# Optimization experiments

Hardware: AMD Instinct MI355X
Metric: run time of the kernel (lower is better)

The kernel has to match this reference:

```python
import jax, jax.numpy as jnp
import numpy as np

N_NODES = 50000
N_EDGES = 800000
IN_FEATS = 128
N_HIDDEN = 128
N_CLASSES = 16


def setup_inputs() -> dict:
    key = jax.random.key(0)
    ks = jax.random.split(key, 10)
    d = {
        'x': jax.random.normal(ks[0], (N_NODES, IN_FEATS), dtype=jnp.float32),
        'src': jax.random.randint(ks[1], (N_EDGES,), 0, N_NODES, dtype=jnp.int32),
        'dst': jax.random.randint(ks[2], (N_EDGES,), 0, N_NODES, dtype=jnp.int32),
    }
    sc = 1.0 / np.sqrt(N_HIDDEN)
    d['w_self0'] = jax.random.normal(ks[3], (IN_FEATS, N_HIDDEN), dtype=jnp.float32) * sc
    d['w_neigh0'] = jax.random.normal(ks[4], (IN_FEATS, N_HIDDEN), dtype=jnp.float32) * sc
    d['b0'] = jnp.zeros((N_HIDDEN,), dtype=jnp.float32)
    d['w_self1'] = jax.random.normal(ks[5], (N_HIDDEN, N_HIDDEN), dtype=jnp.float32) * sc
    d['w_neigh1'] = jax.random.normal(ks[6], (N_HIDDEN, N_HIDDEN), dtype=jnp.float32) * sc
    d['b1'] = jnp.zeros((N_HIDDEN,), dtype=jnp.float32)
    d['w_self2'] = jax.random.normal(ks[7], (N_HIDDEN, N_HIDDEN), dtype=jnp.float32) * sc
    d['w_neigh2'] = jax.random.normal(ks[8], (N_HIDDEN, N_HIDDEN), dtype=jnp.float32) * sc
    d['b2'] = jnp.zeros((N_HIDDEN,), dtype=jnp.float32)
    d['w_head'] = jax.random.normal(ks[9], (N_HIDDEN, N_CLASSES), dtype=jnp.float32) * sc
    d['b_head'] = jnp.zeros((N_CLASSES,), dtype=jnp.float32)
    return d


def _sage_conv(h, src, dst, inv_deg, w_self, w_neigh, b):
    # mean aggregator: gather src features, scatter-add to dst, divide by in-degree
    agg = jax.ops.segment_sum(h[src], dst, num_segments=N_NODES)  # [N, d]
    neigh = agg * inv_deg[:, None]
    return h @ w_self + neigh @ w_neigh + b


def reference(x, src, dst, w_self0, w_neigh0, b0, w_self1, w_neigh1, b1,
              w_self2, w_neigh2, b2, w_head, b_head):
    deg = jax.ops.segment_sum(jnp.ones((src.shape[0],), jnp.float32), dst,
                              num_segments=N_NODES)
    inv_deg = 1.0 / jnp.maximum(deg, 1.0)
    h = x  # dropout is identity in eval mode
    for (ws, wn, b) in ((w_self0, w_neigh0, b0),
                        (w_self1, w_neigh1, b1),
                        (w_self2, w_neigh2, b2)):
        h = jax.nn.relu(_sage_conv(h, src, dst, inv_deg, ws, wn, b))
    pls = jnp.mean(h, axis=0, keepdims=True)  # AvgPooling over single graph -> [1, n_hidden]
    score = pls @ w_head + b_head  # [1, n_classes]
    return (score, pls)
```

## Files before the change

### kernel.cpp

```cpp
#include <hip/hip_runtime.h>
#include <hip/hip_bf16.h>
#include <hip/hip_fp8.h>
#include <stdint.h>

#define NN 50000
#define NE 800000
#define F 128
#define NCLS 16
#define NB 196
#define BCAP 5120
#define PA_EPT 16

typedef __attribute__((ext_vector_type(8))) short short8;
typedef __attribute__((ext_vector_type(4))) float f32x4;
typedef __attribute__((ext_vector_type(2))) float f32x2;
typedef __attribute__((ext_vector_type(4))) unsigned int uint4v;

#define OB_COLSUM    0u
#define OB_BCUR      512u
#define OB_BBASE     1536u
#define OB_ROWSTART  4096u
#define OB_INVDEG    204800u
#define OB_PAIRS     409600u
#define OB_SRCS16    4423680u
#define OB_WT        6023680u
#define OB_XB        6220800u
#define OB_HB1       19020800u
#define OB_X8        31820800u
#define OB_F8A       38220800u
#define OB_NB        44620800u

__device__ __forceinline__ uint32_t swz_off(uint32_t row, uint32_t k) {
    uint32_t c = ((k >> 5) << 2) | ((k >> 2) & 3u);
    uint32_t b = (((k >> 4) & 1u) << 3) | ((k & 3u) << 1);
    return (row << 8) + (((c ^ (row & 15u)) << 4) | b);
}

__device__ __forceinline__ uint32_t pack_bf2(float a, float b) {
    __hip_bfloat16 l = __float2bfloat16(a), h = __float2bfloat16(b);
    return ((uint32_t)(*(uint16_t*)&h) << 16) | (uint32_t)(*(uint16_t*)&l);
}

__device__ __forceinline__ uint8_t f32_to_fp8(float v) {
#if __has_builtin(__builtin_amdgcn_cvt_pk_fp8_f32)
    return (uint8_t)(__builtin_amdgcn_cvt_pk_fp8_f32(v, 0.f, 0, false) & 0xff);
#else
    __hip_fp8_e4m3 t(v);
    return t.__x;
#endif
}

__device__ __forceinline__ uint32_t f32x4_to_fp8x4(float a, float b, float c, float d) {
#if __has_builtin(__builtin_amdgcn_cvt_pk_fp8_f32)
    int r = __builtin_amdgcn_cvt_pk_fp8_f32(a, b, 0, false);
    r = __builtin_amdgcn_cvt_pk_fp8_f32(c, d, r, true);
    return (uint32_t)r;
#else
    __hip_fp8_e4m3 ta(a), tb(b), tc(c), td(d);
    return (uint32_t)ta.__x | ((uint32_t)tb.__x << 8) | ((uint32_t)tc.__x << 16) | ((uint32_t)td.__x << 24);
#endif
}

__device__ __forceinline__ void fp8x4_to_f32(uint32_t d, float& f0, float& f1, float& f2, float& f3) {
#if __has_builtin(__builtin_amdgcn_cvt_pk_f32_fp8)
    f32x2 lo = __builtin_amdgcn_cvt_pk_f32_fp8((int)d, false);
    f32x2 hi = __builtin_amdgcn_cvt_pk_f32_fp8((int)d, true);
    f0 = lo.x; f1 = lo.y; f2 = hi.x; f3 = hi.y;
#else
    __hip_fp8_e4m3 t0, t1, t2, t3;
    t0.__x = (uint8_t)(d & 0xff); t1.__x = (uint8_t)((d >> 8) & 0xff);
    t2.__x = (uint8_t)((d >> 16) & 0xff); t3.__x = (uint8_t)((d >> 24) & 0xff);
    f0 = (float)t0; f1 = (float)t1; f2 = (float)t2; f3 = (float)t3;
#endif
}

__device__ __forceinline__ void gload16(const void* g, void* l) {
    __builtin_amdgcn_global_load_lds(
        (const __attribute__((address_space(1))) unsigned int*)g,
        (__attribute__((address_space(3))) unsigned int*)l, 16, 0, 0);
}

__global__ __launch_bounds__(256) void convert_x2(const float* __restrict__ x,
                                                  uint8_t* __restrict__ xb,
                                                  uint8_t* __restrict__ x8,
                                                  float* __restrict__ colsum,
                                                  int* __restrict__ bcur) {
    if (blockIdx.x == 0) {
        int tt = threadIdx.x;
        if (tt < 128) colsum[tt] = 0.f;
        if (tt < NB) bcur[tt] = tt * BCAP;
    }
    int t = blockIdx.x * 256 + threadIdx.x;
    uint32_t row = (uint32_t)t >> 5;
    uint32_t q = (uint32_t)t & 31u;
    float4 v = *(const float4*)(x + row * F + q * 4);
    uint32_t c = ((q >> 3) << 2) | (q & 3u);
    uint32_t hi = (q >> 2) & 1u;
    uint2 pk;
    pk.x = pack_bf2(v.x, v.y);
    pk.y = pack_bf2(v.z, v.w);
    *(uint2*)(xb + (row << 8) + (((c ^ (row & 15u)) << 4) | (hi << 3))) = pk;
    *(uint32_t*)(x8 + row * 128u + q * 4u) = f32x4_to_fp8x4(v.x, v.y, v.z, v.w);
}

__global__ __launch_bounds__(256) void prep_w(const float* __restrict__ w0, const float* __restrict__ w1,
                                              const float* __restrict__ w2, const float* __restrict__ w3,
                                              const float* __restrict__ w4, const float* __restrict__ w5,
                                              uint8_t* __restrict__ wt) {
    int m = blockIdx.y;
    const float* w = m == 0 ? w0 : m == 1 ? w1 : m == 2 ? w2 : m == 3 ? w3 : m == 4 ? w4 : w5;
    int t = blockIdx.x * 256 + threadIdx.x;
    int n = t >> 6;
    int k0 = (t & 63) << 1;
    uint32_t pk = pack_bf2(w[k0 * F + n], w[(k0 + 1) * F + n]);
    *(uint32_t*)(wt + (uint32_t)m * 32768u + swz_off((uint32_t)n, (uint32_t)k0)) = pk;
}

__global__ __launch_bounds__(256) void pass_a(const int* __restrict__ src,
                                              const int* __restrict__ dst,
                                              int* __restrict__ bcur,
                                              uint32_t* __restrict__ pairs) {
    __shared__ int cnt[NB];
    __shared__ int base_s[NB];
    int t = threadIdx.x;
    for (int i = t; i < NB; i += 256) cnt[i] = 0;
    __syncthreads();

    uint32_t pk[PA_EPT];
    int bk[PA_EPT];
    int e0 = blockIdx.x * (256 * PA_EPT) + t;
#pragma unroll
    for (int j = 0; j < PA_EPT; ++j) {
        int e = e0 + j * 256;
        if (e < NE) {
            int sv = src[e], dv = dst[e];
            bk[j] = dv >> 8;
            pk[j] = (uint32_t)sv | (((uint32_t)dv & 255u) << 16);
            atomicAdd(&cnt[bk[j]], 1);
        } else bk[j] = -1;
    }
    __syncthreads();
    for (int i = t; i < NB; i += 256) {
        if (cnt[i] > 0) base_s[i] = atomicAdd(&bcur[i], cnt[i]);
        cnt[i] = 0;
    }
    __syncthreads();
#pragma unroll
    for (int j = 0; j < PA_EPT; ++j) {
        if (bk[j] >= 0) {
            int pos = base_s[bk[j]] + atomicAdd(&cnt[bk[j]], 1);
            pairs[pos] = pk[j];
        }
    }
}

__global__ __launch_bounds__(256) void bucket_scan(const int* __restrict__ bcur,
                                                   int* __restrict__ bbase,
                                                   int* __restrict__ row_start) {
    __shared__ int s[256];
    int t = threadIdx.x;
    int fill = (t < NB) ? (bcur[t] - t * BCAP) : 0;
    s[t] = fill;
    __syncthreads();
    for (int off = 1; off < 256; off <<= 1) {
        int u = (t >= off) ? s[t - off] : 0;
        __syncthreads();
        s[t] += u;
        __syncthreads();
    }
    if (t < NB) bbase[t] = s[t] - fill;
    if (t == 0) row_start[NN] = NE;
}

__global__ __launch_bounds__(256) void pass_b(const uint32_t* __restrict__ pairs,
                                              const int* __restrict__ bcur,
                                              const int* __restrict__ bbase,
                                              int* __restrict__ row_start,
                                              float* __restrict__ inv_deg,
                                              unsigned short* __restrict__ srcs) {
    __shared__ int cnt[256];
    __shared__ int s[256];
    __shared__ int cur[256];
    int b = blockIdx.x, t = threadIdx.x;
    int in0 = b * BCAP;
    int fill = bcur[b] - in0;
    int out0 = bbase[b];
    cnt[t] = 0;
    __syncthreads();
    for (int i = t; i < fill; i += 256)
        atomicAdd(&cnt[pairs[in0 + i] >> 16], 1);
    __syncthreads();
    int v = cnt[t];
    s[t] = v;
    __syncthreads();
    for (int off = 1; off < 256; off <<= 1) {
        int u = (t >= off) ? s[t - off] : 0;
        __syncthreads();
        s[t] += u;
        __syncthreads();
    }
    int excl = s[t] - v;
    cur[t] = out0 + excl;
    int row = (b << 8) + t;
    if (row < NN) {
        row_start[row] = out0 + excl;
        inv_deg[row] = 1.0f / (float)(v > 1 ? v : 1);
    }
    __syncthreads();
    for (int i = t; i < fill; i += 256) {
        uint32_t p = pairs[in0 + i];
        int pos = atomicAdd(&cur[p >> 16], 1);
        srcs[pos] = (unsigned short)(p & 0xffffu);
    }
}

__global__ __launch_bounds__(256) void aggregate_f8(
        const uint8_t* __restrict__ hf8, const int* __restrict__ row_start,
        const unsigned short* __restrict__ srcs, const float* __restrict__ inv_deg,
        uint8_t* __restrict__ nb) {
    int node = blockIdx.x * 4 + (threadIdx.x >> 6);
    int l = threadIdx.x & 63;
    int g = l >> 4;
    uint32_t m = (uint32_t)(l & 15);
    const uint8_t* base = hf8 + m * 8u;
    int e0 = row_start[node], e1 = row_start[node + 1];
    float a0=0.f,a1=0.f,a2=0.f,a3=0.f,a4=0.f,a5=0.f,a6=0.f,a7=0.f;

    int e = e0 + g;
    for (; e + 4 < e1; e += 8) {
        uint32_t sa = srcs[e];
        uint32_t sb = srcs[e + 4];
        uint2 da = *(const uint2*)(base + ((uint32_t)sa << 7));
        uint2 db = *(const uint2*)(base + ((uint32_t)sb << 7));
        float f0, f1, f2, f3;
        fp8x4_to_f32(da.x, f0,f1,f2,f3); a0+=f0; a1+=f1; a2+=f2; a3+=f3;
        fp8x4_to_f32(da.y, f0,f1,f2,f3); a4+=f0; a5+=f1; a6+=f2; a7+=f3;
        fp8x4_to_f32(db.x, f0,f1,f2,f3); a0+=f0; a1+=f1; a2+=f2; a3+=f3;
        fp8x4_to_f32(db.y, f0,f1,f2,f3); a4+=f0; a5+=f1; a6+=f2; a7+=f3;
    }
    if (e < e1) {
        uint32_t sa = srcs[e];
        uint2 da = *(const uint2*)(base + ((uint32_t)sa << 7));
        float f0, f1, f2, f3;
        fp8x4_to_f32(da.x, f0,f1,f2,f3); a0+=f0; a1+=f1; a2+=f2; a3+=f3;
        fp8x4_to_f32(da.y, f0,f1,f2,f3); a4+=f0; a5+=f1; a6+=f2; a7+=f3;
    }
    a0 += __shfl_xor(a0, 16); a1 += __shfl_xor(a1, 16);
    a2 += __shfl_xor(a2, 16); a3 += __shfl_xor(a3, 16);
    a4 += __shfl_xor(a4, 16); a5 += __shfl_xor(a5, 16);
    a6 += __shfl_xor(a6, 16); a7 += __shfl_xor(a7, 16);
    a0 += __shfl_xor(a0, 32); a1 += __shfl_xor(a1, 32);
    a2 += __shfl_xor(a2, 32); a3 += __shfl_xor(a3, 32);
    a4 += __shfl_xor(a4, 32); a5 += __shfl_xor(a5, 32);
    a6 += __shfl_xor(a6, 32); a7 += __shfl_xor(a7, 32);

    if (g == 0) {
        float idg = inv_deg[node];
        uint2 w0, w1;
        w0.x = pack_bf2(a0 * idg, a1 * idg);
        w0.y = pack_bf2(a2 * idg, a3 * idg);
        w1.x = pack_bf2(a4 * idg, a5 * idg);
        w1.y = pack_bf2(a6 * idg, a7 * idg);
        uint32_t c1 = m >> 2;
        uint32_t h  = (m >> 1) & 1u;
        uint32_t ca = (c1 << 2) | ((2u * m) & 3u);
        uint32_t cb = (c1 << 2) | ((2u * m + 1u) & 3u);
        uint32_t rx = (uint32_t)node & 15u;
        char* rowp = (char*)nb + ((uint32_t)node << 8);
        *(uint2*)(rowp + (((ca ^ rx) << 4) | (h << 3))) = w0;
        *(uint2*)(rowp + (((cb ^ rx) << 4) | (h << 3))) = w1;
    }
}

__global__ __launch_bounds__(256) void gemm_mfma(
        const uint8_t* __restrict__ a_self, const uint8_t* __restrict__ a_neigh,
        const uint8_t* __restrict__ wt_self, const uint8_t* __restrict__ wt_neigh,
        const float* __restrict__ bias, uint8_t* __restrict__ hout,
        uint8_t* hout_f8, float* colsum) {
    __shared__ uint4v As4[1024];
    __shared__ uint4v Ws4[2048];
    __shared__ float cs[128];
    int tid = threadIdx.x;
    int lane = tid & 63, wave = tid >> 6;
    int rl = lane & 15, g = lane >> 4;
    int row0 = blockIdx.x * 64;

    f32x4 acc[8];
    f32x4 z = {0.f, 0.f, 0.f, 0.f};
#pragma unroll
    for (int nt = 0; nt < 8; ++nt) acc[nt] = z;

    const char* AsB = (const char*)As4;
    const char* WsB = (const char*)Ws4;

#pragma unroll
    for (int pass = 0; pass < 2; ++pass) {
        if (pass) __syncthreads();
        const uint4v* ga = (const uint4v*)((pass ? a_neigh : a_self) + (size_t)row0 * 256);
        const uint4v* gw = (const uint4v*)(pass ? wt_neigh : wt_self);
#pragma unroll
        for (int i = 0; i < 4; ++i) gload16(&ga[tid + i * 256], &As4[tid + i * 256]);
#pragma unroll
        for (int i = 0; i < 8; ++i) gload16(&gw[tid + i * 256], &Ws4[tid + i * 256]);
        __syncthreads();
#pragma unroll
        for (int ks = 0; ks < 4; ++ks) {
            int chunk = ((ks << 2) | g) ^ rl;
            short8 a = *(const short8*)(AsB + ((wave * 16 + rl) << 8) + (chunk << 4));
#pragma unroll
            for (int nt = 0; nt < 8; ++nt) {
                short8 bb = *(const short8*)(WsB + ((nt * 16 + rl) << 8) + (chunk << 4));
                acc[nt] = __builtin_amdgcn_mfma_f32_16x16x32_bf16(a, bb, acc[nt], 0, 0, 0);
            }
        }
    }

    bool doCol = (colsum != nullptr);
    bool doF8 = (hout_f8 != nullptr);
    if (doCol) {
        if (tid < 128) cs[tid] = 0.f;
        __syncthreads();
    }
#pragma unroll
    for (int nt = 0; nt < 8; ++nt) {
        int col = nt * 16 + rl;
        float bv = bias[col];
        float rsum = 0.f;
#pragma unroll
        for (int i = 0; i < 4; ++i) {
            int row = row0 + wave * 16 + g * 4 + i;
            if (row < NN) {
                float v = fmaxf(acc[nt][i] + bv, 0.f);
                rsum += v;
                *(__hip_bfloat16*)(hout + swz_off((uint32_t)row, (uint32_t)col)) =
                    __float2bfloat16(v);
                if (doF8) hout_f8[(uint32_t)row * 128u + (uint32_t)col] = f32_to_fp8(v);
            }
        }
        if (doCol) atomicAdd(&cs[col], rsum);
    }
    if (doCol) {
        __syncthreads();
        if (tid < 128) atomicAdd(&colsum[tid], cs[tid]);
    }
}

__global__ __launch_bounds__(128) void head_kernel(const float* __restrict__ colsum,
                                                   const float* __restrict__ w_head,
                                                   const float* __restrict__ b_head,
                                                   float* __restrict__ out) {
    __shared__ float pls[F];
    int t = threadIdx.x;
    float p = colsum[t] * (1.0f / (float)NN);
    pls[t] = p;
    out[NCLS + t] = p;
    __syncthreads();
    if (t < NCLS) {
        float sc = b_head[t];
        for (int f = 0; f < F; ++f) sc += pls[f] * w_head[f * NCLS + t];
        out[t] = sc;
    }
}

extern "C" void kernel_launch(void* const* d_in, const int* in_sizes, int n_in,
                              void* d_out, int out_size, void* d_ws, size_t ws_size,
                              hipStream_t stream) {
    const float* x       = (const float*)d_in[0];
    const int*   src     = (const int*)d_in[1];
    const int*   dst     = (const int*)d_in[2];
    const float* w_self0 = (const float*)d_in[3];
    const float* w_neigh0= (const float*)d_in[4];
    const float* b0      = (const float*)d_in[5];
    const float* w_self1 = (const float*)d_in[6];
    const float* w_neigh1= (const float*)d_in[7];
    const float* b1      = (const float*)d_in[8];
    const float* w_self2 = (const float*)d_in[9];
    const float* w_neigh2= (const float*)d_in[10];
    const float* b2      = (const float*)d_in[11];
    const float* w_head  = (const float*)d_in[12];
    const float* b_head  = (const float*)d_in[13];
    float* out = (float*)d_out;

    uint8_t* ws = (uint8_t*)d_ws;
    float* colsum   = (float*)(ws + OB_COLSUM);
    int*   bcur     = (int*)(ws + OB_BCUR);
    int*   bbase    = (int*)(ws + OB_BBASE);
    int*   row_start= (int*)(ws + OB_ROWSTART);
    float* inv_deg  = (float*)(ws + OB_INVDEG);
    uint32_t* pairs = (uint32_t*)(ws + OB_PAIRS);
    unsigned short* srcs16 = (unsigned short*)(ws + OB_SRCS16);
    uint8_t* wt     = ws + OB_WT;
    uint8_t* xb     = ws + OB_XB;
    uint8_t* hb1    = ws + OB_HB1;
    uint8_t* x8     = ws + OB_X8;
    uint8_t* f8a    = ws + OB_F8A;
    uint8_t* nb     = ws + OB_NB;

    convert_x2<<<6250, 256, 0, stream>>>(x, xb, x8, colsum, bcur);
    prep_w<<<dim3(32, 6), 256, 0, stream>>>(w_self0, w_neigh0, w_self1, w_neigh1,
                                            w_self2, w_neigh2, wt);
    pass_a<<<NB, 256, 0, stream>>>(src, dst, bcur, pairs);
    bucket_scan<<<1, 256, 0, stream>>>(bcur, bbase, row_start);
    pass_b<<<NB, 256, 0, stream>>>(pairs, bcur, bbase, row_start, inv_deg, srcs16);

    const int GB = (NN + 63) / 64;

    aggregate_f8<<<12500, 256, 0, stream>>>(x8, row_start, srcs16, inv_deg, nb);
    gemm_mfma<<<GB, 256, 0, stream>>>(xb, nb, wt + 0 * 32768, wt + 1 * 32768, b0,
                                      hb1, f8a, nullptr);
    aggregate_f8<<<12500, 256, 0, stream>>>(f8a, row_start, srcs16, inv_deg, nb);
    gemm_mfma<<<GB, 256, 0, stream>>>(hb1, nb, wt + 2 * 32768, wt + 3 * 32768, b1,
                                      xb, x8, nullptr);
    aggregate_f8<<<12500, 256, 0, stream>>>(x8, row_start, srcs16, inv_deg, nb);
    gemm_mfma<<<GB, 256, 0, stream>>>(xb, nb, wt + 4 * 32768, wt + 5 * 32768, b2,
                                      hb1, nullptr, colsum);

    head_kernel<<<1, 128, 0, stream>>>(colsum, w_head, b_head, out);
}
```

Before: 198.9 us.

## Fuse preprocessing kernels, fold bucket scan into pass_b, widen aggregate loads

Merges the x conversion, weight packing and edge bucketing kernels into one launch, with a memset zeroing colsum and the bucket counters. The separate bucket scan kernel is removed: every pass_b block now recomputes the bucket prefix sum itself. The aggregate kernel switches to 8 lanes per edge with 16-byte fp8 loads and packed f32x2 accumulation, processing more edges per iteration. This cuts launch count and gather instruction count, at the cost of redundant scans per block and more shuffle reduction steps.

Result: slower. 204.3 us (+2.7%).

```diff
diff --git a/kernel.cpp b/kernel.cpp
--- a/kernel.cpp
+++ b/kernel.cpp
@@ -10,6 +10,8 @@
 #define NB 196
 #define BCAP 5120
 #define PA_EPT 16
+#define PW_BLKS 192
+#define CV_BLKS 6250
 
 typedef __attribute__((ext_vector_type(8))) short short8;
 typedef __attribute__((ext_vector_type(4))) float f32x4;
@@ -18,7 +20,6 @@
 
 #define OB_COLSUM    0u
 #define OB_BCUR      512u
-#define OB_BBASE     1536u
 #define OB_ROWSTART  4096u
 #define OB_INVDEG    204800u
 #define OB_PAIRS     409600u
@@ -61,16 +62,15 @@
 #endif
 }
 
-__device__ __forceinline__ void fp8x4_to_f32(uint32_t d, float& f0, float& f1, float& f2, float& f3) {
+__device__ __forceinline__ void acc4(uint32_t d, f32x2& p0, f32x2& p1) {
 #if __has_builtin(__builtin_amdgcn_cvt_pk_f32_fp8)
-    f32x2 lo = __builtin_amdgcn_cvt_pk_f32_fp8((int)d, false);
-    f32x2 hi = __builtin_amdgcn_cvt_pk_f32_fp8((int)d, true);
-    f0 = lo.x; f1 = lo.y; f2 = hi.x; f3 = hi.y;
+    p0 += __builtin_amdgcn_cvt_pk_f32_fp8((int)d, false);
+    p1 += __builtin_amdgcn_cvt_pk_f32_fp8((int)d, true);
 #else
     __hip_fp8_e4m3 t0, t1, t2, t3;
     t0.__x = (uint8_t)(d & 0xff); t1.__x = (uint8_t)((d >> 8) & 0xff);
     t2.__x = (uint8_t)((d >> 16) & 0xff); t3.__x = (uint8_t)((d >> 24) & 0xff);
-    f0 = (float)t0; f1 = (float)t1; f2 = (float)t2; f3 = (float)t3;
+    p0.x += (float)t0; p0.y += (float)t1; p1.x += (float)t2; p1.y += (float)t3;
 #endif
 }
 
@@ -80,19 +80,65 @@
         (__attribute__((address_space(3))) unsigned int*)l, 16, 0, 0);
 }
 
-__global__ __launch_bounds__(256) void convert_x2(const float* __restrict__ x,
-                                                  uint8_t* __restrict__ xb,
-                                                  uint8_t* __restrict__ x8,
-                                                  float* __restrict__ colsum,
-                                                  int* __restrict__ bcur) {
-    if (blockIdx.x == 0) {
-        int tt = threadIdx.x;
-        if (tt < 128) colsum[tt] = 0.f;
-        if (tt < NB) bcur[tt] = tt * BCAP;
-    }
-    int t = blockIdx.x * 256 + threadIdx.x;
-    uint32_t row = (uint32_t)t >> 5;
-    uint32_t q = (uint32_t)t & 31u;
+__global__ __launch_bounds__(256) void fused_prep(
+        const float* __restrict__ x, uint8_t* __restrict__ xb, uint8_t* __restrict__ x8,
+        const float* __restrict__ w0, const float* __restrict__ w1,
+        const float* __restrict__ w2, const float* __restrict__ w3,
+        const float* __restrict__ w4, const float* __restrict__ w5,
+        uint8_t* __restrict__ wt,
+        const int* __restrict__ src, const int* __restrict__ dst,
+        int* __restrict__ bcur, uint32_t* __restrict__ pairs) {
+    __shared__ int cnt[NB];
+    __shared__ int base_s[NB];
+    int bid = blockIdx.x;
+    int t = threadIdx.x;
+
+    if (bid < NB) {
+        for (int i = t; i < NB; i += 256) cnt[i] = 0;
+        __syncthreads();
+        uint32_t pk[PA_EPT];
+        int bk[PA_EPT];
+        int e0 = bid * (256 * PA_EPT) + t;
+#pragma unroll
+        for (int j = 0; j < PA_EPT; ++j) {
+            int e = e0 + j * 256;
+            if (e < NE) {
+                int sv = src[e], dv = dst[e];
+                bk[j] = dv >> 8;
+                pk[j] = (uint32_t)sv | (((uint32_t)dv & 255u) << 16);
+                atomicAdd(&cnt[bk[j]], 1);
+            } else bk[j] = -1;
+        }
+        __syncthreads();
+        for (int i = t; i < NB; i += 256) {
+            if (cnt[i] > 0) base_s[i] = i * BCAP + atomicAdd(&bcur[i], cnt[i]);
+            cnt[i] = 0;
+        }
+        __syncthreads();
+#pragma unroll
+        for (int j = 0; j < PA_EPT; ++j) {
+            if (bk[j] >= 0) {
+                int pos = base_s[bk[j]] + atomicAdd(&cnt[bk[j]], 1);
+                pairs[pos] = pk[j];
+            }
+        }
+        return;
+    }
+    bid -= NB;
+    if (bid < PW_BLKS) {
+        int m = bid >> 5;
+        const float* w = m == 0 ? w0 : m == 1 ? w1 : m == 2 ? w2 : m == 3 ? w3 : m == 4 ? w4 : w5;
+        int tt = (bid & 31) * 256 + t;
+        int n = tt >> 6;
+        int k0 = (tt & 63) << 1;
+        uint32_t pk = pack_bf2(w[k0 * F + n], w[(k0 + 1) * F + n]);
+        *(uint32_t*)(wt + (uint32_t)m * 32768u + swz_off((uint32_t)n, (uint32_t)k0)) = pk;
+        return;
+    }
+    bid -= PW_BLKS;
+    int tt = bid * 256 + t;
+    uint32_t row = (uint32_t)tt >> 5;
+    uint32_t q = (uint32_t)tt & 31u;
     float4 v = *(const float4*)(x + row * F + q * 4);
     uint32_t c = ((q >> 3) << 2) | (q & 3u);
     uint32_t hi = (q >> 2) & 1u;
@@ -103,109 +149,48 @@
     *(uint32_t*)(x8 + row * 128u + q * 4u) = f32x4_to_fp8x4(v.x, v.y, v.z, v.w);
 }
 
-__global__ __launch_bounds__(256) void prep_w(const float* __restrict__ w0, const float* __restrict__ w1,
-                                              const float* __restrict__ w2, const float* __restrict__ w3,
-                                              const float* __restrict__ w4, const float* __restrict__ w5,
-                                              uint8_t* __restrict__ wt) {
-    int m = blockIdx.y;
-    const float* w = m == 0 ? w0 : m == 1 ? w1 : m == 2 ? w2 : m == 3 ? w3 : m == 4 ? w4 : w5;
-    int t = blockIdx.x * 256 + threadIdx.x;
-    int n = t >> 6;
-    int k0 = (t & 63) << 1;
-    uint32_t pk = pack_bf2(w[k0 * F + n], w[(k0 + 1) * F + n]);
-    *(uint32_t*)(wt + (uint32_t)m * 32768u + swz_off((uint32_t)n, (uint32_t)k0)) = pk;
-}
-
-__global__ __launch_bounds__(256) void pass_a(const int* __restrict__ src,
-                                              const int* __restrict__ dst,
-                                              int* __restrict__ bcur,
-                                              uint32_t* __restrict__ pairs) {
-    __shared__ int cnt[NB];
-    __shared__ int base_s[NB];
-    int t = threadIdx.x;
-    for (int i = t; i < NB; i += 256) cnt[i] = 0;
-    __syncthreads();
-
-    uint32_t pk[PA_EPT];
-    int bk[PA_EPT];
-    int e0 = blockIdx.x * (256 * PA_EPT) + t;
-#pragma unroll
-    for (int j = 0; j < PA_EPT; ++j) {
-        int e = e0 + j * 256;
-        if (e < NE) {
-            int sv = src[e], dv = dst[e];
-            bk[j] = dv >> 8;
-            pk[j] = (uint32_t)sv | (((uint32_t)dv & 255u) << 16);
-            atomicAdd(&cnt[bk[j]], 1);
-        } else bk[j] = -1;
-    }
-    __syncthreads();
-    for (int i = t; i < NB; i += 256) {
-        if (cnt[i] > 0) base_s[i] = atomicAdd(&bcur[i], cnt[i]);
-        cnt[i] = 0;
-    }
-    __syncthreads();
-#pragma unroll
-    for (int j = 0; j < PA_EPT; ++j) {
-        if (bk[j] >= 0) {
-            int pos = base_s[bk[j]] + atomicAdd(&cnt[bk[j]], 1);
-            pairs[pos] = pk[j];
-        }
-    }
-}
-
-__global__ __launch_bounds__(256) void bucket_scan(const int* __restrict__ bcur,
-                                                   int* __restrict__ bbase,
-                                                   int* __restrict__ row_start) {
-    __shared__ int s[256];
-    int t = threadIdx.x;
-    int fill = (t < NB) ? (bcur[t] - t * BCAP) : 0;
-    s[t] = fill;
-    __syncthreads();
-    for (int off = 1; off < 256; off <<= 1) {
-        int u = (t >= off) ? s[t - off] : 0;
-        __syncthreads();
-        s[t] += u;
-        __syncthreads();
-    }
-    if (t < NB) bbase[t] = s[t] - fill;
-    if (t == 0) row_start[NN] = NE;
-}
-
 __global__ __launch_bounds__(256) void pass_b(const uint32_t* __restrict__ pairs,
                                               const int* __restrict__ bcur,
-                                              const int* __restrict__ bbase,
                                               int* __restrict__ row_start,
                                               float* __restrict__ inv_deg,
                                               unsigned short* __restrict__ srcs) {
+    __shared__ int sarr[256];
     __shared__ int cnt[256];
-    __shared__ int s[256];
     __shared__ int cur[256];
     int b = blockIdx.x, t = threadIdx.x;
+    sarr[t] = (t < NB) ? bcur[t] : 0;
+    __syncthreads();
+    for (int off = 1; off < 256; off <<= 1) {
+        int u = (t >= off) ? sarr[t - off] : 0;
+        __syncthreads();
+        sarr[t] += u;
+        __syncthreads();
+    }
+    int fill = bcur[b];
+    int out0 = sarr[b] - fill;
     int in0 = b * BCAP;
-    int fill = bcur[b] - in0;
-    int out0 = bbase[b];
     cnt[t] = 0;
     __syncthreads();
     for (int i = t; i < fill; i += 256)
         atomicAdd(&cnt[pairs[in0 + i] >> 16], 1);
     __syncthreads();
     int v = cnt[t];
-    s[t] = v;
+    sarr[t] = v;
     __syncthreads();
     for (int off = 1; off < 256; off <<= 1) {
-        int u = (t >= off) ? s[t - off] : 0;
-        __syncthreads();
-        s[t] += u;
-        __syncthreads();
-    }
-    int excl = s[t] - v;
+        int u = (t >= off) ? sarr[t - off] : 0;
+        __syncthreads();
+        sarr[t] += u;
+        __syncthreads();
+    }
+    int excl = sarr[t] - v;
     cur[t] = out0 + excl;
     int row = (b << 8) + t;
     if (row < NN) {
         row_start[row] = out0 + excl;
         inv_deg[row] = 1.0f / (float)(v > 1 ? v : 1);
     }
+    if (b == 0 && t == 0) row_start[NN] = NE;
     __syncthreads();
     for (int i = t; i < fill; i += 256) {
         uint32_t p = pairs[in0 + i];
@@ -220,55 +205,59 @@
         uint8_t* __restrict__ nb) {
     int node = blockIdx.x * 4 + (threadIdx.x >> 6);
     int l = threadIdx.x & 63;
-    int g = l >> 4;
-    uint32_t m = (uint32_t)(l & 15);
-    const uint8_t* base = hf8 + m * 8u;
+    int g = l >> 3;
+    uint32_t m = (uint32_t)(l & 7);
+    const uint8_t* base = hf8 + m * 16u;
     int e0 = row_start[node], e1 = row_start[node + 1];
-    float a0=0.f,a1=0.f,a2=0.f,a3=0.f,a4=0.f,a5=0.f,a6=0.f,a7=0.f;
-
-    int e = e0 + g;
-    for (; e + 4 < e1; e += 8) {
-        uint32_t sa = srcs[e];
-        uint32_t sb = srcs[e + 4];
-        uint2 da = *(const uint2*)(base + ((uint32_t)sa << 7));
-        uint2 db = *(const uint2*)(base + ((uint32_t)sb << 7));
-        float f0, f1, f2, f3;
-        fp8x4_to_f32(da.x, f0,f1,f2,f3); a0+=f0; a1+=f1; a2+=f2; a3+=f3;
-        fp8x4_to_f32(da.y, f0,f1,f2,f3); a4+=f0; a5+=f1; a6+=f2; a7+=f3;
-        fp8x4_to_f32(db.x, f0,f1,f2,f3); a0+=f0; a1+=f1; a2+=f2; a3+=f3;
-        fp8x4_to_f32(db.y, f0,f1,f2,f3); a4+=f0; a5+=f1; a6+=f2; a7+=f3;
-    }
-    if (e < e1) {
-        uint32_t sa = srcs[e];
-        uint2 da = *(const uint2*)(base + ((uint32_t)sa << 7));
-        float f0, f1, f2, f3;
-        fp8x4_to_f32(da.x, f0,f1,f2,f3); a0+=f0; a1+=f1; a2+=f2; a3+=f3;
-        fp8x4_to_f32(da.y, f0,f1,f2,f3); a4+=f0; a5+=f1; a6+=f2; a7+=f3;
-    }
-    a0 += __shfl_xor(a0, 16); a1 += __shfl_xor(a1, 16);
-    a2 += __shfl_xor(a2, 16); a3 += __shfl_xor(a3, 16);
-    a4 += __shfl_xor(a4, 16); a5 += __shfl_xor(a5, 16);
-    a6 += __shfl_xor(a6, 16); a7 += __shfl_xor(a7, 16);
-    a0 += __shfl_xor(a0, 32); a1 += __shfl_xor(a1, 32);
-    a2 += __shfl_xor(a2, 32); a3 += __shfl_xor(a3, 32);
-    a4 += __shfl_xor(a4, 32); a5 += __shfl_xor(a5, 32);
-    a6 += __shfl_xor(a6, 32); a7 += __shfl_xor(a7, 32);
-
+    f32x2 a[8];
+#pragma unroll
+    for (int i = 0; i < 8; ++i) { a[i].x = 0.f; a[i].y = 0.f; }
+
+    int e = e0;
+    for (; e + 16 <= e1; e += 16) {
+        uint32_t sa = srcs[e + g];
+        uint32_t sb = srcs[e + 8 + g];
+        uint4 da = *(const uint4*)(base + ((uint32_t)sa << 7));
+        uint4 db = *(const uint4*)(base + ((uint32_t)sb << 7));
+        acc4(da.x, a[0], a[1]); acc4(da.y, a[2], a[3]);
+        acc4(da.z, a[4], a[5]); acc4(da.w, a[6], a[7]);
+        acc4(db.x, a[0], a[1]); acc4(db.y, a[2], a[3]);
+        acc4(db.z, a[4], a[5]); acc4(db.w, a[6], a[7]);
+    }
+    if (e + 8 <= e1) {
+        uint32_t sa = srcs[e + g];
+        uint4 da = *(const uint4*)(base + ((uint32_t)sa << 7));
+        acc4(da.x, a[0], a[1]); acc4(da.y, a[2], a[3]);
+        acc4(da.z, a[4], a[5]); acc4(da.w, a[6], a[7]);
+        e += 8;
+    }
+    if (e + g < e1) {
+        uint32_t sa = srcs[e + g];
+        uint4 da = *(const uint4*)(base + ((uint32_t)sa << 7));
+        acc4(da.x, a[0], a[1]); acc4(da.y, a[2], a[3]);
+        acc4(da.z, a[4], a[5]); acc4(da.w, a[6], a[7]);
+    }
+#pragma unroll
+    for (int d = 8; d < 64; d <<= 1) {
+#pragma unroll
+        for (int i = 0; i < 8; ++i) {
+            a[i].x += __shfl_xor(a[i].x, d);
+            a[i].y += __shfl_xor(a[i].y, d);
+        }
+    }
     if (g == 0) {
         float idg = inv_deg[node];
-        uint2 w0, w1;
-        w0.x = pack_bf2(a0 * idg, a1 * idg);
-        w0.y = pack_bf2(a2 * idg, a3 * idg);
-        w1.x = pack_bf2(a4 * idg, a5 * idg);
-        w1.y = pack_bf2(a6 * idg, a7 * idg);
-        uint32_t c1 = m >> 2;
-        uint32_t h  = (m >> 1) & 1u;
-        uint32_t ca = (c1 << 2) | ((2u * m) & 3u);
-        uint32_t cb = (c1 << 2) | ((2u * m + 1u) & 3u);
         uint32_t rx = (uint32_t)node & 15u;
         char* rowp = (char*)nb + ((uint32_t)node << 8);
-        *(uint2*)(rowp + (((ca ^ rx) << 4) | (h << 3))) = w0;
-        *(uint2*)(rowp + (((cb ^ rx) << 4) | (h << 3))) = w1;
+        uint32_t bh = (m & 1u) << 3;
+#pragma unroll
+        for (int jj = 0; jj < 4; ++jj) {
+            uint32_t c = ((m >> 1) << 2) | (uint32_t)jj;
+            uint2 w;
+            w.x = pack_bf2(a[2 * jj].x * idg, a[2 * jj].y * idg);
+            w.y = pack_bf2(a[2 * jj + 1].x * idg, a[2 * jj + 1].y * idg);
+            *(uint2*)(rowp + (((c ^ rx) << 4) | bh)) = w;
+        }
     }
 }
 
@@ -384,7 +373,6 @@
     uint8_t* ws = (uint8_t*)d_ws;
     float* colsum   = (float*)(ws + OB_COLSUM);
     int*   bcur     = (int*)(ws + OB_BCUR);
-    int*   bbase    = (int*)(ws + OB_BBASE);
     int*   row_start= (int*)(ws + OB_ROWSTART);
     float* inv_deg  = (float*)(ws + OB_INVDEG);
     uint32_t* pairs = (uint32_t*)(ws + OB_PAIRS);
@@ -396,12 +384,12 @@
     uint8_t* f8a    = ws + OB_F8A;
     uint8_t* nb     = ws + OB_NB;
 
-    convert_x2<<<6250, 256, 0, stream>>>(x, xb, x8, colsum, bcur);
-    prep_w<<<dim3(32, 6), 256, 0, stream>>>(w_self0, w_neigh0, w_self1, w_neigh1,
-                                            w_self2, w_neigh2, wt);
-    pass_a<<<NB, 256, 0, stream>>>(src, dst, bcur, pairs);
-    bucket_scan<<<1, 256, 0, stream>>>(bcur, bbase, row_start);
-    pass_b<<<NB, 256, 0, stream>>>(pairs, bcur, bbase, row_start, inv_deg, srcs16);
+    hipMemsetAsync(d_ws, 0, 1536, stream);
+
+    fused_prep<<<NB + PW_BLKS + CV_BLKS, 256, 0, stream>>>(
+        x, xb, x8, w_self0, w_neigh0, w_self1, w_neigh1, w_self2, w_neigh2, wt,
+        src, dst, bcur, pairs);
+    pass_b<<<NB, 256, 0, stream>>>(pairs, bcur, row_start, inv_deg, srcs16);
 
     const int GB = (NN + 63) / 64;
 
```
